# Optimization experiments

Measured on AMD Instinct MI355X. Metric: run time of the kernel, lower is better.

The kernel has to match this reference:

```python
import jax, jax.numpy as jnp
import numpy as np

SMALL = -1000.0


def setup_inputs() -> dict:
    key = jax.random.key(0)
    k1, k2, k3, k4 = jax.random.split(key, 4)
    B, T, L = 256, 1024, 64
    pred = jax.random.normal(k1, (B, T, L), dtype=jnp.float32)
    seq_len = jax.random.randint(k2, (B,), T // 2, T + 1)  # lengths in [T/2, T]
    ref = jax.random.randint(k3, (B, T), 0, L)
    # zero-pad tags beyond seq_len (required by the original end-tag indexing trick)
    ref = jnp.where(jnp.arange(T)[None, :] < seq_len[:, None], ref, 0)
    transitions = jax.random.normal(k4, (L + 2, L + 2), dtype=jnp.float32) * 0.1
    return {"pred": pred, "transitions": transitions, "ref": ref, "seq_len": seq_len}


def crf_neg_log_likelihood(pred, transitions, ref, seq_len):
    B, T, L = pred.shape
    dt = pred.dtype
    # --- build padded observations [B, T+2, L+2] ---
    obs_mid = jnp.concatenate([pred, jnp.full((B, T, 2), SMALL, dt)], axis=2)
    b_s = jnp.concatenate([jnp.full((L,), SMALL), jnp.array([0.0, SMALL])]).astype(dt)
    r_p = jnp.concatenate([jnp.zeros((L,)), jnp.array([SMALL, SMALL])]).astype(dt)
    obs = jnp.concatenate(
        [jnp.broadcast_to(b_s, (B, 1, L + 2)), obs_mid, jnp.broadcast_to(r_p, (B, 1, L + 2))],
        axis=1,
    )
    e_s = jnp.concatenate([jnp.full((L,), SMALL), jnp.array([0.0, 1000.0])]).astype(dt)
    obs = obs.at[jnp.arange(B), seq_len + 1].add(e_s)

    # --- forward algorithm: logsumexp recurrence over time ---
    def step(prev, ob):  # prev [B, L+2], ob [B, L+2]
        new = jax.nn.logsumexp(prev[:, :, None] + ob[:, None, :] + transitions[None], axis=1)
        return new, new

    prev0 = obs[:, 0]
    obs_t = jnp.swapaxes(obs[:, 1:], 0, 1)  # [T+1, B, L+2] time-major
    _, paths = jax.lax.scan(step, prev0, obs_t)  # paths [T+1, B, L+2]
    all_paths_scores = jax.nn.logsumexp(paths[seq_len, jnp.arange(B)], axis=1).sum()

    # --- gold path score ---
    mask = (jnp.arange(T)[None, :] < seq_len[:, None]).astype(dt)
    gold_emit = jnp.sum(jnp.take_along_axis(pred, ref[..., None], axis=2)[..., 0] * mask)
    padded = jnp.concatenate(
        [jnp.full((B, 1), L, ref.dtype), ref, jnp.zeros((B, 1), ref.dtype)], axis=1
    )  # [B, T+2]
    padded = padded.at[jnp.arange(B), seq_len + 1].add(L + 1)  # end tag id = L+1
    trans_sc = transitions[padded[:, :-1], padded[:, 1:]]  # [B, T+1]
    mask2 = (jnp.arange(T + 1)[None, :] < (seq_len + 1)[:, None]).astype(dt)
    gold = gold_emit + jnp.sum(trans_sc * mask2)
    return all_paths_scores - gold


def reference(pred, transitions, ref, seq_len):
    return crf_neg_log_likelihood(pred, transitions, ref, seq_len)
```

## Files before the change

### kernel.cpp

```cpp
#include <hip/hip_runtime.h>
#include <hip/hip_bf16.h>
#include <hip/hip_fp16.h>


typedef _Float16 h2 __attribute__((ext_vector_type(2)));
#define B2U(x) __builtin_bit_cast(unsigned, x)
#define U2H(x) __builtin_bit_cast(h2, x)
#define L2E 1.44269504088896340736f
#define LN2 0.69314718055994530942f
#define EXPE(p) __builtin_amdgcn_exp2f((p) * L2E)
#define SBAR __builtin_amdgcn_sched_barrier(0)

#define W_ALL(M) M(0) M(1) M(2) M(3) M(4) M(5) M(6) M(7) M(8) M(9) M(10) M(11) \
 M(12) M(13) M(14) M(15) M(16) M(17) M(18) M(19) M(20) M(21) M(22) M(23) M(24) \
 M(25) M(26) M(27) M(28) M(29) M(30) M(31)

#define DECLW(q) unsigned W##q;
#define LOADF(q) W##q = B2U(__builtin_amdgcn_cvt_pkrtz(EXPE(tcol[(2*(q))*66]), EXPE(tcol[(2*(q)+1)*66])));
#define LOADB(q) W##q = B2U(__builtin_amdgcn_cvt_pkrtz(EXPE(trow[2*(q)]), EXPE(trow[2*(q)+1])));
#define PINW(q)  asm volatile("" : "+v"(W##q));

#define RLD(q) int u##q = __builtin_amdgcn_readlane((int)P, 2*(q));
#define RL16A RLD(0) RLD(1) RLD(2) RLD(3) RLD(4) RLD(5) RLD(6) RLD(7) \
              RLD(8) RLD(9) RLD(10) RLD(11) RLD(12) RLD(13) RLD(14) RLD(15)
#define RL16B RLD(16) RLD(17) RLD(18) RLD(19) RLD(20) RLD(21) RLD(22) RLD(23) \
              RLD(24) RLD(25) RLD(26) RLD(27) RLD(28) RLD(29) RLD(30) RLD(31)

#if __has_builtin(__builtin_amdgcn_fdot2)
#define DOTQ(q, acc) acc = __builtin_amdgcn_fdot2(U2H((unsigned)u##q), U2H(W##q), acc, false);
#else
#define DOTQ(q, acc) { h2 _u = U2H((unsigned)u##q), _w = U2H(W##q); \
    acc = fmaf((float)_u[0], (float)_w[0], fmaf((float)_u[1], (float)_w[1], acc)); }
#endif
#define DOT16A \
    DOTQ(0,s0)  DOTQ(1,s1)  DOTQ(2,s2)  DOTQ(3,s3)  DOTQ(4,s0)  DOTQ(5,s1) \
    DOTQ(6,s2)  DOTQ(7,s3)  DOTQ(8,s0)  DOTQ(9,s1)  DOTQ(10,s2) DOTQ(11,s3) \
    DOTQ(12,s0) DOTQ(13,s1) DOTQ(14,s2) DOTQ(15,s3)
#define DOT16B \
    DOTQ(16,s0) DOTQ(17,s1) DOTQ(18,s2) DOTQ(19,s3) DOTQ(20,s0) DOTQ(21,s1) \
    DOTQ(22,s2) DOTQ(23,s3) DOTQ(24,s0) DOTQ(25,s1) DOTQ(26,s2) DOTQ(27,s3) \
    DOTQ(28,s0) DOTQ(29,s1) DOTQ(30,s2) DOTQ(31,s3)

#define ROWF(i) pb[(((i) < 0) ? 0 : (((i) > 1023) ? 1023 : (i))) * 64]

#define DPPSWAP(x) __uint_as_float((unsigned)__builtin_amdgcn_mov_dpp( \
    (int)__float_as_uint(x), 0xB1, 0xF, 0xF, true))

#define STEPX(E) { \
    unsigned abits = (unsigned)__builtin_amdgcn_readfirstlane((int)__float_as_uint(a)); \
    int k = (int)((abits >> 23) & 255u) - 122; \
    K += k; \
    float sc = __uint_as_float((unsigned)(127 - k) << 23); \
    float x = FWD ? a * sc : (a * sc) * (E); \
    float xo = DPPSWAP(x); \
    unsigned P = B2U(__builtin_amdgcn_cvt_pkrtz(x, xo)); \
    float s0 = 0.f, s1 = 0.f, s2 = 0.f, s3 = 0.f; \
    RL16A \
    SBAR; \
    DOT16A \
    RL16B \
    SBAR; \
    DOT16B \
    float s = (s0 + s1) + (s2 + s3); \
    a = FWD ? s * (E) : s; }

template<bool FWD>
__device__ __forceinline__ void chain(const float* __restrict__ pred,
                                      const float* __restrict__ trans,
                                      int b, int lane, int sl, int h,
                                      float* __restrict__ wsV,
                                      int* __restrict__ wsK)
{
    const float* pb   = pred + (size_t)b * 65536 + lane;
    const float* tcol = trans + lane;
    const float* trow = trans + lane * 66;
    (void)tcol; (void)trow;

    W_ALL(DECLW)
    if (FWD) { W_ALL(LOADF) } else { W_ALL(LOADB) }
    W_ALL(PINW)

    float a;
    int   K = 0;
    if (FWD) a = __builtin_amdgcn_exp2f((pb[0] + trans[64 * 66 + lane]) * L2E);
    else     a = __builtin_amdgcn_exp2f(trow[65] * L2E);

    const int dir = FWD ? 1 : -1;
    int n = FWD ? h - 1 : sl - h;
    int r = FWD ? 1 : sl - 1;

    float E0 = EXPE(ROWF(r)), E1 = EXPE(ROWF(r + dir)),
          E2 = EXPE(ROWF(r + 2 * dir)), E3 = EXPE(ROWF(r + 3 * dir));
    while (n >= 4) {
        float F0 = ROWF(r + 4 * dir), F1 = ROWF(r + 5 * dir),
              F2 = ROWF(r + 6 * dir), F3 = ROWF(r + 7 * dir);
        STEPX(E0) STEPX(E1) STEPX(E2) STEPX(E3)
        E0 = EXPE(F0); E1 = EXPE(F1); E2 = EXPE(F2); E3 = EXPE(F3);
        r += 4 * dir; n -= 4;
    }
    if (n > 0) { STEPX(E0) --n; }
    if (n > 0) { STEPX(E1) --n; }
    if (n > 0) { STEPX(E2) }

    wsV[b * 64 + lane] = a;
    if (lane == 0) wsK[b] = K;
}

__global__ __launch_bounds__(64) __attribute__((amdgpu_waves_per_eu(1, 1)))
void chain_kernel(const float* __restrict__ pred,
                  const float* __restrict__ trans,
                  const int*   __restrict__ ref,
                  const int*   __restrict__ seqlen,
                  float* __restrict__ wsA, float* __restrict__ wsB,
                  int* __restrict__ wsKf, int* __restrict__ wsKb,
                  float* __restrict__ out)
{
    const int role = blockIdx.x >> 8;
    const int b    = blockIdx.x & 255;
    const int lane = threadIdx.x;
    const int sl   = seqlen[b];
    const int h    = (sl + 1) >> 1;

    if (role == 0) {
        chain<true>(pred, trans, b, lane, sl, h, wsA, wsKf);
    } else if (role == 1) {
        chain<false>(pred, trans, b, lane, sl, h, wsB, wsKb);
    } else {
        const int*   rb = ref  + b * 1024;
        const float* pg = pred + (size_t)b * 65536;
        float acc = 0.f;
        for (int t = lane; t <= sl; t += 64) {
            int from = (t == 0) ? 64 : rb[t - 1];
            int cur  = (t < sl) ? rb[t] : 65;
            acc += trans[from * 66 + cur];
            if (t < sl) acc += pg[t * 64 + cur];
        }
        #pragma unroll
        for (int off = 32; off; off >>= 1) acc += __shfl_xor(acc, off, 64);
        if (lane == 0) atomicAdd(out, -acc);
    }
}

__global__ __launch_bounds__(64) void combine_kernel(
    const float* __restrict__ wsA, const float* __restrict__ wsB,
    const int* __restrict__ wsKf, const int* __restrict__ wsKb,
    float* __restrict__ out)
{
    const int b = blockIdx.x, lane = threadIdx.x;
    float z = wsA[b * 64 + lane] * wsB[b * 64 + lane];
    #pragma unroll
    for (int off = 32; off; off >>= 1) z += __shfl_xor(z, off, 64);
    if (lane == 0) {
        float res = LN2 * (__builtin_amdgcn_logf(z) + (float)(wsKf[b] + wsKb[b]));
        atomicAdd(out, res);
    }
}

extern "C" void kernel_launch(void* const* d_in, const int* in_sizes, int n_in,
                              void* d_out, int out_size, void* d_ws, size_t ws_size,
                              hipStream_t stream) {
    const float* pred   = (const float*)d_in[0];
    const float* trans  = (const float*)d_in[1];
    const int*   ref    = (const int*)d_in[2];
    const int*   seqlen = (const int*)d_in[3];
    float* out = (float*)d_out;

    float* wsA  = (float*)d_ws;
    float* wsB  = wsA + 256 * 64;
    int*   wsKf = (int*)(wsB + 256 * 64);
    int*   wsKb = wsKf + 256;

    hipMemsetAsync(out, 0, sizeof(float), stream);
    chain_kernel<<<768, 64, 0, stream>>>(pred, trans, ref, seqlen,
                                         wsA, wsB, wsKf, wsKb, out);
    combine_kernel<<<256, 64, 0, stream>>>(wsA, wsB, wsKf, wsKb, out);
}
```

Before: 182.0 us.

## Split CRF forward chain into parallel 128-step transfer-matrix segments via MFMA

Instead of a forward and a backward chain each covering half the sequence, the sequence is cut into 128-step segments. The middle segments are computed in parallel as products of 64x64 exp-transition matrices using fp16 MFMA, with per-step power-of-two rescaling. The forward chain covers the first 128 steps and the backward chain covers the tail. The combine kernel then chains the segment matrices as matrix-vector products. This shortens the serial dependency chain from about sl/2 steps to about 128, but adds matrix-matrix work, fp16 precision loss in the matrix products, and workspace traffic.

```diff
diff --git a/kernel.cpp b/kernel.cpp
--- a/kernel.cpp
+++ b/kernel.cpp
@@ -4,12 +4,18 @@
 
 
 typedef _Float16 h2 __attribute__((ext_vector_type(2)));
+typedef _Float16 half8 __attribute__((ext_vector_type(8)));
+typedef float f32x16 __attribute__((ext_vector_type(16)));
+typedef unsigned u32x2 __attribute__((ext_vector_type(2)));
+typedef unsigned u32x4 __attribute__((ext_vector_type(4)));
+
 #define B2U(x) __builtin_bit_cast(unsigned, x)
 #define U2H(x) __builtin_bit_cast(h2, x)
 #define L2E 1.44269504088896340736f
 #define LN2 0.69314718055994530942f
 #define EXPE(p) __builtin_amdgcn_exp2f((p) * L2E)
 #define SBAR __builtin_amdgcn_sched_barrier(0)
+
 
 #define W_ALL(M) M(0) M(1) M(2) M(3) M(4) M(5) M(6) M(7) M(8) M(9) M(10) M(11) \
  M(12) M(13) M(14) M(15) M(16) M(17) M(18) M(19) M(20) M(21) M(22) M(23) M(24) \
@@ -106,26 +112,135 @@
     if (lane == 0) wsK[b] = K;
 }
 
-__global__ __launch_bounds__(64) __attribute__((amdgpu_waves_per_eu(1, 1)))
+
+#define MFMA16(a, b, c) __builtin_amdgcn_mfma_f32_32x32x16_f16(a, b, c, 0, 0, 0)
+
+#define PACKGRP(Csrc, base, dst) { \
+    unsigned q0 = B2U(__builtin_amdgcn_cvt_pkrtz(Csrc[(base)+0], Csrc[(base)+1])); \
+    unsigned q2 = B2U(__builtin_amdgcn_cvt_pkrtz(Csrc[(base)+2], Csrc[(base)+3])); \
+    unsigned q4 = B2U(__builtin_amdgcn_cvt_pkrtz(Csrc[(base)+4], Csrc[(base)+5])); \
+    unsigned q6 = B2U(__builtin_amdgcn_cvt_pkrtz(Csrc[(base)+6], Csrc[(base)+7])); \
+    asm("v_permlane32_swap_b32 %0, %1" : "+v"(q0), "+v"(q4)); \
+    asm("v_permlane32_swap_b32 %0, %1" : "+v"(q2), "+v"(q6)); \
+    u32x4 qv = {q0, q2, q4, q6}; \
+    dst = __builtin_bit_cast(half8, qv); }
+
+#define STORET(Ct, t4) { \
+    _Pragma("unroll") \
+    for (int g = 0; g < 4; ++g) { \
+        u32x2 pv; \
+        pv.x = B2U(__builtin_amdgcn_cvt_pkrtz(Ct[4*g+0], Ct[4*g+1])); \
+        pv.y = B2U(__builtin_amdgcn_cvt_pkrtz(Ct[4*g+2], Ct[4*g+3])); \
+        *(u32x2*)(wm + (t4)*1024 + g*256 + lane*4) = pv; } }
+
+__device__ __forceinline__ void midseg(const float* __restrict__ pred,
+                                       const float* __restrict__ trans,
+                                       int b, int lane, int sl, int s,
+                                       _Float16* __restrict__ wsM,
+                                       int* __restrict__ wsKm)
+{
+    const int nm = (sl - 128) >> 7;
+    if (s >= nm) return;
+    const int t0 = 128 * (1 + s);
+    const int H  = lane >> 5;
+    const int j0 = lane & 31;
+
+    half8 VA[2][4];
+    #pragma unroll
+    for (int mt = 0; mt < 2; ++mt)
+        #pragma unroll
+        for (int s4 = 0; s4 < 4; ++s4) {
+            half8 va;
+            #pragma unroll
+            for (int e = 0; e < 8; ++e) {
+                int k = 16 * s4 + 8 * H + e;
+                va[e] = (_Float16)EXPE(trans[k * 66 + 32 * mt + j0]);
+            }
+            VA[mt][s4] = va;
+        }
+
+    half8 Bf[4][2];
+    #pragma unroll
+    for (int s4 = 0; s4 < 4; ++s4)
+        #pragma unroll
+        for (int nt = 0; nt < 2; ++nt) {
+            half8 bb;
+            #pragma unroll
+            for (int e = 0; e < 8; ++e)
+                bb[e] = (16 * s4 + 8 * H + e == 32 * nt + j0) ? (_Float16)1.f
+                                                              : (_Float16)0.f;
+            Bf[s4][nt] = bb;
+        }
+
+    const float* pp = pred + (size_t)b * 65536 + j0;
+    float a0 = pp[(size_t)t0 * 64],        a1 = pp[(size_t)t0 * 64 + 32];
+    float q0 = pp[(size_t)(t0 + 1) * 64],  q1 = pp[(size_t)(t0 + 1) * 64 + 32];
+
+    const f32x16 Z16 = {0.f,0.f,0.f,0.f,0.f,0.f,0.f,0.f,
+                        0.f,0.f,0.f,0.f,0.f,0.f,0.f,0.f};
+    f32x16 C00 = Z16, C01 = Z16, C10 = Z16, C11 = Z16;
+    int   K   = 0;
+    float scf = 1.0f;
+
+    for (int i = 0; i < 128; ++i) {
+        int tn = t0 + i + 2; if (tn > 1023) tn = 1023;
+        float n0 = pp[(size_t)tn * 64], n1 = pp[(size_t)tn * 64 + 32];
+
+        if (i > 0) {
+            float sr = ((C00[0]+C00[1])+(C00[2]+C00[3]))+((C00[4]+C00[5])+(C00[6]+C00[7]))
+                     + ((C00[8]+C00[9])+(C00[10]+C00[11]))+((C00[12]+C00[13])+(C00[14]+C00[15]));
+            unsigned cb = (unsigned)__builtin_amdgcn_readfirstlane((int)__float_as_uint(sr));
+            int kk = (int)((cb >> 23) & 255u) - 129;
+            K += kk;
+            scf = __uint_as_float((unsigned)(127 - kk) << 23);
+            PACKGRP(C00, 0, Bf[0][0]) PACKGRP(C00, 8, Bf[1][0])
+            PACKGRP(C10, 0, Bf[2][0]) PACKGRP(C10, 8, Bf[3][0])
+            PACKGRP(C01, 0, Bf[0][1]) PACKGRP(C01, 8, Bf[1][1])
+            PACKGRP(C11, 0, Bf[2][1]) PACKGRP(C11, 8, Bf[3][1])
+        }
+        float e0 = EXPE(a0) * scf, e1 = EXPE(a1) * scf;
+        _Float16 h0 = (_Float16)e0, h1 = (_Float16)e1;
+        half8 E0v = {h0,h0,h0,h0,h0,h0,h0,h0};
+        half8 E1v = {h1,h1,h1,h1,h1,h1,h1,h1};
+        half8 A00 = VA[0][0]*E0v, A01 = VA[0][1]*E0v, A02 = VA[0][2]*E0v, A03 = VA[0][3]*E0v;
+        half8 A10 = VA[1][0]*E1v, A11 = VA[1][1]*E1v, A12 = VA[1][2]*E1v, A13 = VA[1][3]*E1v;
+
+        C00 = MFMA16(A00, Bf[0][0], MFMA16(A01, Bf[1][0], MFMA16(A02, Bf[2][0], MFMA16(A03, Bf[3][0], Z16))));
+        C01 = MFMA16(A00, Bf[0][1], MFMA16(A01, Bf[1][1], MFMA16(A02, Bf[2][1], MFMA16(A03, Bf[3][1], Z16))));
+        C10 = MFMA16(A10, Bf[0][0], MFMA16(A11, Bf[1][0], MFMA16(A12, Bf[2][0], MFMA16(A13, Bf[3][0], Z16))));
+        C11 = MFMA16(A10, Bf[0][1], MFMA16(A11, Bf[1][1], MFMA16(A12, Bf[2][1], MFMA16(A13, Bf[3][1], Z16))));
+
+        a0 = q0; a1 = q1; q0 = n0; q1 = n1;
+    }
+
+    _Float16* wm = wsM + (size_t)(b * 7 + s) * 4096;
+    STORET(C00, 0) STORET(C01, 1) STORET(C10, 2) STORET(C11, 3)
+    if (lane == 0) wsKm[b * 7 + s] = K;
+}
+
+
+__global__ __launch_bounds__(64) __attribute__((amdgpu_waves_per_eu(2)))
 void chain_kernel(const float* __restrict__ pred,
                   const float* __restrict__ trans,
                   const int*   __restrict__ ref,
                   const int*   __restrict__ seqlen,
                   float* __restrict__ wsA, float* __restrict__ wsB,
                   int* __restrict__ wsKf, int* __restrict__ wsKb,
+                  _Float16* __restrict__ wsM, int* __restrict__ wsKm,
                   float* __restrict__ out)
 {
     const int role = blockIdx.x >> 8;
     const int b    = blockIdx.x & 255;
     const int lane = threadIdx.x;
     const int sl   = seqlen[b];
-    const int h    = (sl + 1) >> 1;
 
     if (role == 0) {
-        chain<true>(pred, trans, b, lane, sl, h, wsA, wsKf);
+        chain<true>(pred, trans, b, lane, sl, 128, wsA, wsKf);
     } else if (role == 1) {
-        chain<false>(pred, trans, b, lane, sl, h, wsB, wsKb);
-    } else {
+        const int nm = (sl - 128) >> 7;
+        const int tb = 128 * (1 + nm);
+        chain<false>(pred, trans, b, lane, sl, tb, wsB, wsKb);
+    } else if (role == 2) {
         const int*   rb = ref  + b * 1024;
         const float* pg = pred + (size_t)b * 65536;
         float acc = 0.f;
@@ -138,20 +253,50 @@
         #pragma unroll
         for (int off = 32; off; off >>= 1) acc += __shfl_xor(acc, off, 64);
         if (lane == 0) atomicAdd(out, -acc);
+    } else {
+        midseg(pred, trans, b, lane, sl, role - 3, wsM, wsKm);
     }
 }
 
 __global__ __launch_bounds__(64) void combine_kernel(
     const float* __restrict__ wsA, const float* __restrict__ wsB,
+    const _Float16* __restrict__ wsM,
     const int* __restrict__ wsKf, const int* __restrict__ wsKb,
+    const int* __restrict__ wsKm, const int* __restrict__ seqlen,
     float* __restrict__ out)
 {
-    const int b = blockIdx.x, lane = threadIdx.x;
-    float z = wsA[b * 64 + lane] * wsB[b * 64 + lane];
+    const int b = blockIdx.x, j = threadIdx.x;
+    const int sl = seqlen[b];
+    const int nm = (sl - 128) >> 7;
+
+    float v = wsA[b * 64 + j];
+    int   K = wsKf[b] + wsKb[b];
+
+    const int mt = j >> 5, hi = (j >> 2) & 1, g = (j >> 3) & 3, e = j & 3;
+    const _Float16* mb = wsM + (size_t)b * 7 * 4096 + mt * 2048 + g * 256 + hi * 128 + e;
+
+    for (int s = 0; s < nm; ++s) {
+        K += wsKm[b * 7 + s];
+        const _Float16* ms = mb + (size_t)s * 4096;
+        float acc = 0.f;
+        #pragma unroll
+        for (int c = 0; c < 64; ++c) {
+            float m  = (float)ms[(c >> 5) * 1024 + (c & 31) * 4];
+            float vc = __uint_as_float(
+                (unsigned)__builtin_amdgcn_readlane((int)__float_as_uint(v), c));
+            acc = fmaf(m, vc, acc);
+        }
+        unsigned ab = (unsigned)__builtin_amdgcn_readfirstlane((int)__float_as_uint(acc));
+        int k2 = (int)((ab >> 23) & 255u) - 127;
+        K += k2;
+        v = acc * __uint_as_float((unsigned)(127 - k2) << 23);
+    }
+
+    float z = v * wsB[b * 64 + j];
     #pragma unroll
     for (int off = 32; off; off >>= 1) z += __shfl_xor(z, off, 64);
-    if (lane == 0) {
-        float res = LN2 * (__builtin_amdgcn_logf(z) + (float)(wsKf[b] + wsKb[b]));
+    if (j == 0) {
+        float res = LN2 * (__builtin_amdgcn_logf(z) + (float)K);
         atomicAdd(out, res);
     }
 }
@@ -169,9 +314,12 @@
     float* wsB  = wsA + 256 * 64;
     int*   wsKf = (int*)(wsB + 256 * 64);
     int*   wsKb = wsKf + 256;
+    int*   wsKm = wsKb + 256;
+    _Float16* wsM = (_Float16*)(wsKm + 256 * 7);
 
     hipMemsetAsync(out, 0, sizeof(float), stream);
-    chain_kernel<<<768, 64, 0, stream>>>(pred, trans, ref, seqlen,
-                                         wsA, wsB, wsKf, wsKb, out);
-    combine_kernel<<<256, 64, 0, stream>>>(wsA, wsB, wsKf, wsKb, out);
-}
+    chain_kernel<<<2560, 64, 0, stream>>>(pred, trans, ref, seqlen,
+                                          wsA, wsB, wsKf, wsKb, wsM, wsKm, out);
+    combine_kernel<<<256, 64, 0, stream>>>(wsA, wsB, wsM, wsKf, wsKb, wsKm,
+                                           seqlen, out);
+}
```

New measurement: 227.3 us. +24.9%, slower.

## Split CRF forward chain into parallel MFMA transfer-matrix segments

Applied to the files above, without the earlier changes.

The forward chain now covers only the first G steps and the backward chain only the tail. The middle is cut into segments of G steps, and each segment gets its own block. That block computes a 64x64 transfer-matrix product with fp16 MFMA, rescaling by exponent each step. A combine kernel then chains the segment matrices with the forward vector. This replaces the long serial per-batch recurrence with parallel segments that are serial only over G. In exchange it adds heavier matrix-matrix work, an fp16 precision risk, and a larger workspace, with a fallback configuration when the workspace is too small.

```diff
diff --git a/kernel.cpp b/kernel.cpp
--- a/kernel.cpp
+++ b/kernel.cpp
@@ -4,12 +4,18 @@
 
 
 typedef _Float16 h2 __attribute__((ext_vector_type(2)));
+typedef _Float16 half4v __attribute__((ext_vector_type(4)));
+typedef float f32x4 __attribute__((ext_vector_type(4)));
+typedef unsigned u32x2 __attribute__((ext_vector_type(2)));
+typedef unsigned u32x4 __attribute__((ext_vector_type(4)));
+
 #define B2U(x) __builtin_bit_cast(unsigned, x)
 #define U2H(x) __builtin_bit_cast(h2, x)
 #define L2E 1.44269504088896340736f
 #define LN2 0.69314718055994530942f
 #define EXPE(p) __builtin_amdgcn_exp2f((p) * L2E)
 #define SBAR __builtin_amdgcn_sched_barrier(0)
+
 
 #define W_ALL(M) M(0) M(1) M(2) M(3) M(4) M(5) M(6) M(7) M(8) M(9) M(10) M(11) \
  M(12) M(13) M(14) M(15) M(16) M(17) M(18) M(19) M(20) M(21) M(22) M(23) M(24) \
@@ -106,26 +112,155 @@
     if (lane == 0) wsK[b] = K;
 }
 
-__global__ __launch_bounds__(64) __attribute__((amdgpu_waves_per_eu(1, 1)))
+
+#define MF16(a, b, c) __builtin_amdgcn_mfma_f32_16x16x16f16(a, b, c, 0, 0, 0)
+
+#define MKE(es) __builtin_bit_cast(half4v, (u32x2){ \
+    B2U(__builtin_amdgcn_cvt_pkrtz((es), (es))), \
+    B2U(__builtin_amdgcn_cvt_pkrtz((es), (es))) })
+
+#define MBROW(mb, EV) { \
+    half4v A0 = VA[mb][0]*(EV), A1 = VA[mb][1]*(EV), \
+           A2 = VA[mb][2]*(EV), A3 = VA[mb][3]*(EV); \
+    _Pragma("unroll") \
+    for (int nb = 0; nb < 4; ++nb) { \
+        f32x4 acc = {0.f, 0.f, 0.f, 0.f}; \
+        acc = MF16(A0, Bf[0][nb], acc); \
+        acc = MF16(A1, Bf[1][nb], acc); \
+        acc = MF16(A2, Bf[2][nb], acc); \
+        acc = MF16(A3, Bf[3][nb], acc); \
+        Cn[mb][nb] = acc; } }
+
+template<int LOGG, int NSLOT>
+__device__ __forceinline__ void midseg(const float* __restrict__ pred,
+                                       const float* __restrict__ trans,
+                                       int b, int lane, int sl, int s,
+                                       _Float16* __restrict__ wsM,
+                                       int* __restrict__ wsKm)
+{
+    const int G  = 1 << LOGG;
+    const int nm = (sl - G) >> LOGG;
+    if (s >= nm) return;
+    const int t0 = G * (1 + s);
+    const int H  = lane >> 4;
+    const int j0 = lane & 15;
+
+    half4v VA[4][4];
+    #pragma unroll
+    for (int mb = 0; mb < 4; ++mb)
+        #pragma unroll
+        for (int kb = 0; kb < 4; ++kb) {
+            const float* tp = trans + (16*kb + 4*H) * 66 + 16*mb + j0;
+            u32x2 q;
+            q.x = B2U(__builtin_amdgcn_cvt_pkrtz(EXPE(tp[0]),   EXPE(tp[66])));
+            q.y = B2U(__builtin_amdgcn_cvt_pkrtz(EXPE(tp[132]), EXPE(tp[198])));
+            VA[mb][kb] = __builtin_bit_cast(half4v, q);
+        }
+
+    half4v Bf[4][4];
+    #pragma unroll
+    for (int kb = 0; kb < 4; ++kb)
+        #pragma unroll
+        for (int nb = 0; nb < 4; ++nb) {
+            half4v bb;
+            #pragma unroll
+            for (int e = 0; e < 4; ++e)
+                bb[e] = (16*kb + 4*H + e == 16*nb + j0) ? (_Float16)1.f
+                                                        : (_Float16)0.f;
+            Bf[kb][nb] = bb;
+        }
+
+    const float* pp = pred + (size_t)b * 65536 + j0;
+    float eA0 = EXPE(pp[(size_t)t0*64]),      eA1 = EXPE(pp[(size_t)t0*64+16]),
+          eA2 = EXPE(pp[(size_t)t0*64+32]),   eA3 = EXPE(pp[(size_t)t0*64+48]);
+    float eB0 = EXPE(pp[(size_t)(t0+1)*64]),    eB1 = EXPE(pp[(size_t)(t0+1)*64+16]),
+          eB2 = EXPE(pp[(size_t)(t0+1)*64+32]), eB3 = EXPE(pp[(size_t)(t0+1)*64+48]);
+
+    f32x4 C[4][4];
+    #pragma unroll
+    for (int mb = 0; mb < 4; ++mb)
+        #pragma unroll
+        for (int nb = 0; nb < 4; ++nb)
+            C[mb][nb] = (f32x4){0.f, 0.f, 0.f, 0.f};
+
+    int   K   = 0;
+    float scf = 1.0f;
+
+    for (int i = 0; i < G; ++i) {
+        int tn = t0 + i + 2; if (tn > 1023) tn = 1023;
+        float g0 = pp[(size_t)tn*64],    g1 = pp[(size_t)tn*64+16],
+              g2 = pp[(size_t)tn*64+32], g3 = pp[(size_t)tn*64+48];
+
+        if (i > 0) {
+            float sr = ((C[0][0][0]+C[0][0][1])+(C[0][0][2]+C[0][0][3]))
+                     + ((C[1][0][0]+C[1][0][1])+(C[1][0][2]+C[1][0][3]))
+                     + ((C[2][0][0]+C[2][0][1])+(C[2][0][2]+C[2][0][3]))
+                     + ((C[3][0][0]+C[3][0][1])+(C[3][0][2]+C[3][0][3]));
+            unsigned cb = (unsigned)__builtin_amdgcn_readfirstlane((int)__float_as_uint(sr));
+            int kk = (int)((cb >> 23) & 255u) - 129;
+            K += kk;
+            scf = __uint_as_float((unsigned)(127 - kk) << 23);
+            #pragma unroll
+            for (int kb = 0; kb < 4; ++kb)
+                #pragma unroll
+                for (int nb = 0; nb < 4; ++nb) {
+                    u32x2 q;
+                    q.x = B2U(__builtin_amdgcn_cvt_pkrtz(C[kb][nb][0], C[kb][nb][1]));
+                    q.y = B2U(__builtin_amdgcn_cvt_pkrtz(C[kb][nb][2], C[kb][nb][3]));
+                    Bf[kb][nb] = __builtin_bit_cast(half4v, q);
+                }
+        }
+
+        float es0 = eA0*scf, es1 = eA1*scf, es2 = eA2*scf, es3 = eA3*scf;
+        half4v E0 = MKE(es0), E1 = MKE(es1), E2 = MKE(es2), E3 = MKE(es3);
+
+        f32x4 Cn[4][4];
+        MBROW(0, E0) MBROW(1, E1) MBROW(2, E2) MBROW(3, E3)
+        #pragma unroll
+        for (int mb = 0; mb < 4; ++mb)
+            #pragma unroll
+            for (int nb = 0; nb < 4; ++nb)
+                C[mb][nb] = Cn[mb][nb];
+
+        eA0 = eB0; eA1 = eB1; eA2 = eB2; eA3 = eB3;
+        eB0 = EXPE(g0); eB1 = EXPE(g1); eB2 = EXPE(g2); eB3 = EXPE(g3);
+    }
+
+    _Float16* wm = wsM + ((size_t)b * NSLOT + s) * 4096;
+    #pragma unroll
+    for (int mb = 0; mb < 4; ++mb)
+        #pragma unroll
+        for (int nb = 0; nb < 4; ++nb)
+            #pragma unroll
+            for (int r = 0; r < 4; ++r)
+                wm[(16*mb + 4*H + r) * 64 + 16*nb + j0] = (_Float16)C[mb][nb][r];
+    if (lane == 0) wsKm[b * NSLOT + s] = K;
+}
+
+
+template<int LOGG, int NSLOT>
+__global__ __launch_bounds__(64)
 void chain_kernel(const float* __restrict__ pred,
                   const float* __restrict__ trans,
                   const int*   __restrict__ ref,
                   const int*   __restrict__ seqlen,
                   float* __restrict__ wsA, float* __restrict__ wsB,
                   int* __restrict__ wsKf, int* __restrict__ wsKb,
+                  _Float16* __restrict__ wsM, int* __restrict__ wsKm,
                   float* __restrict__ out)
 {
     const int role = blockIdx.x >> 8;
     const int b    = blockIdx.x & 255;
     const int lane = threadIdx.x;
     const int sl   = seqlen[b];
-    const int h    = (sl + 1) >> 1;
+    const int G    = 1 << LOGG;
 
     if (role == 0) {
-        chain<true>(pred, trans, b, lane, sl, h, wsA, wsKf);
+        chain<true>(pred, trans, b, lane, sl, G, wsA, wsKf);
     } else if (role == 1) {
-        chain<false>(pred, trans, b, lane, sl, h, wsB, wsKb);
-    } else {
+        const int nm = (sl - G) >> LOGG;
+        chain<false>(pred, trans, b, lane, sl, G * (1 + nm), wsB, wsKb);
+    } else if (role == 2) {
         const int*   rb = ref  + b * 1024;
         const float* pg = pred + (size_t)b * 65536;
         float acc = 0.f;
@@ -138,22 +273,80 @@
         #pragma unroll
         for (int off = 32; off; off >>= 1) acc += __shfl_xor(acc, off, 64);
         if (lane == 0) atomicAdd(out, -acc);
-    }
-}
-
+    } else {
+        midseg<LOGG, NSLOT>(pred, trans, b, lane, sl, role - 3, wsM, wsKm);
+    }
+}
+
+template<int LOGG, int NSLOT>
 __global__ __launch_bounds__(64) void combine_kernel(
     const float* __restrict__ wsA, const float* __restrict__ wsB,
+    const _Float16* __restrict__ wsM,
     const int* __restrict__ wsKf, const int* __restrict__ wsKb,
+    const int* __restrict__ wsKm, const int* __restrict__ seqlen,
     float* __restrict__ out)
 {
-    const int b = blockIdx.x, lane = threadIdx.x;
-    float z = wsA[b * 64 + lane] * wsB[b * 64 + lane];
+    const int b = blockIdx.x, j = threadIdx.x;
+    const int sl = seqlen[b];
+    const int nm = (sl - (1 << LOGG)) >> LOGG;
+
+    float v = wsA[b * 64 + j];
+    int   K = wsKf[b] + wsKb[b];
+    const _Float16* mrow = wsM + (size_t)b * NSLOT * 4096 + j * 64;
+
+    for (int s = 0; s < nm; ++s) {
+        K += wsKm[b * NSLOT + s];
+        const u32x4* mp = (const u32x4*)(mrow + (size_t)s * 4096);
+        u32x4 L0 = mp[0], L1 = mp[1], L2 = mp[2], L3 = mp[3],
+              L4 = mp[4], L5 = mp[5], L6 = mp[6], L7 = mp[7];
+        unsigned mw[32] = {L0.x,L0.y,L0.z,L0.w, L1.x,L1.y,L1.z,L1.w,
+                           L2.x,L2.y,L2.z,L2.w, L3.x,L3.y,L3.z,L3.w,
+                           L4.x,L4.y,L4.z,L4.w, L5.x,L5.y,L5.z,L5.w,
+                           L6.x,L6.y,L6.z,L6.w, L7.x,L7.y,L7.z,L7.w};
+        float av[4] = {0.f, 0.f, 0.f, 0.f};
+        #pragma unroll
+        for (int q = 0; q < 32; ++q) {
+            h2 p = U2H(mw[q]);
+            float v0 = __uint_as_float((unsigned)
+                __builtin_amdgcn_readlane((int)__float_as_uint(v), 2*q));
+            float v1 = __uint_as_float((unsigned)
+                __builtin_amdgcn_readlane((int)__float_as_uint(v), 2*q + 1));
+            av[q & 3] = fmaf((float)p[0], v0, fmaf((float)p[1], v1, av[q & 3]));
+        }
+        float acc = (av[0] + av[1]) + (av[2] + av[3]);
+        unsigned ab = (unsigned)__builtin_amdgcn_readfirstlane((int)__float_as_uint(acc));
+        int k2 = (int)((ab >> 23) & 255u) - 127;
+        K += k2;
+        v = acc * __uint_as_float((unsigned)(127 - k2) << 23);
+    }
+
+    float z = v * wsB[b * 64 + j];
     #pragma unroll
     for (int off = 32; off; off >>= 1) z += __shfl_xor(z, off, 64);
-    if (lane == 0) {
-        float res = LN2 * (__builtin_amdgcn_logf(z) + (float)(wsKf[b] + wsKb[b]));
+    if (j == 0) {
+        float res = LN2 * (__builtin_amdgcn_logf(z) + (float)K);
         atomicAdd(out, res);
     }
+}
+
+
+template<int LOGG, int NSLOT>
+static void launch_all(const float* pred, const float* trans, const int* ref,
+                       const int* seqlen, float* out, void* d_ws,
+                       hipStream_t stream)
+{
+    float* wsA  = (float*)d_ws;
+    float* wsB  = wsA + 256 * 64;
+    int*   wsKf = (int*)(wsB + 256 * 64);
+    int*   wsKb = wsKf + 256;
+    int*   wsKm = wsKb + 256;
+    _Float16* wsM = (_Float16*)(wsKm + 256 * NSLOT);
+
+    hipMemsetAsync(out, 0, sizeof(float), stream);
+    chain_kernel<LOGG, NSLOT><<<256 * (3 + NSLOT), 64, 0, stream>>>(
+        pred, trans, ref, seqlen, wsA, wsB, wsKf, wsKb, wsM, wsKm, out);
+    combine_kernel<LOGG, NSLOT><<<256, 64, 0, stream>>>(
+        wsA, wsB, wsM, wsKf, wsKb, wsKm, seqlen, out);
 }
 
 extern "C" void kernel_launch(void* const* d_in, const int* in_sizes, int n_in,
@@ -165,13 +358,10 @@
     const int*   seqlen = (const int*)d_in[3];
     float* out = (float*)d_out;
 
-    float* wsA  = (float*)d_ws;
-    float* wsB  = wsA + 256 * 64;
-    int*   wsKf = (int*)(wsB + 256 * 64);
-    int*   wsKb = wsKf + 256;
-
-    hipMemsetAsync(out, 0, sizeof(float), stream);
-    chain_kernel<<<768, 64, 0, stream>>>(pred, trans, ref, seqlen,
-                                         wsA, wsB, wsKf, wsKb, out);
-    combine_kernel<<<256, 64, 0, stream>>>(wsA, wsB, wsKf, wsKb, out);
-}
+    const size_t need64 = 2*65536 + 2*1024 + (size_t)256*15*4
+                        + (size_t)256*15*4096*2;
+    if (ws_size >= need64)
+        launch_all<6, 15>(pred, trans, ref, seqlen, out, d_ws, stream);
+    else
+        launch_all<7, 7>(pred, trans, ref, seqlen, out, d_ws, stream);
+}
```

Measured after the change: 255.1 us. +40.2%, slower.

## Replace readlane/fdot2 recurrence with MFMA 16x16x32 matrix-vector steps

Applied to the files above, without the earlier changes.

The per-step 64x64 matrix-vector product of the forward/backward CRF chains is now computed with MFMA f16 instructions. exp(transitions) is held as A fragments, and the state vector is broadcast as a B operand with identical columns. This removes the 32 readlane plus 32 fdot2 sequence per step, but adds MFMA latency on the serial dependency chain. The scaling now uses a sum of the 16 per-lane state values, and the emissions are loaded as float4 slices in the MFMA output layout.

```diff
diff --git a/kernel.cpp b/kernel.cpp
--- a/kernel.cpp
+++ b/kernel.cpp
@@ -1,108 +1,138 @@
 #include <hip/hip_runtime.h>
-#include <hip/hip_bf16.h>
 #include <hip/hip_fp16.h>
 
 
 typedef _Float16 h2 __attribute__((ext_vector_type(2)));
+typedef _Float16 half8 __attribute__((ext_vector_type(8)));
+typedef float f32x4 __attribute__((ext_vector_type(4)));
+typedef unsigned u32x4 __attribute__((ext_vector_type(4)));
+
 #define B2U(x) __builtin_bit_cast(unsigned, x)
-#define U2H(x) __builtin_bit_cast(h2, x)
 #define L2E 1.44269504088896340736f
 #define LN2 0.69314718055994530942f
 #define EXPE(p) __builtin_amdgcn_exp2f((p) * L2E)
-#define SBAR __builtin_amdgcn_sched_barrier(0)
-
-#define W_ALL(M) M(0) M(1) M(2) M(3) M(4) M(5) M(6) M(7) M(8) M(9) M(10) M(11) \
- M(12) M(13) M(14) M(15) M(16) M(17) M(18) M(19) M(20) M(21) M(22) M(23) M(24) \
- M(25) M(26) M(27) M(28) M(29) M(30) M(31)
-
-#define DECLW(q) unsigned W##q;
-#define LOADF(q) W##q = B2U(__builtin_amdgcn_cvt_pkrtz(EXPE(tcol[(2*(q))*66]), EXPE(tcol[(2*(q)+1)*66])));
-#define LOADB(q) W##q = B2U(__builtin_amdgcn_cvt_pkrtz(EXPE(trow[2*(q)]), EXPE(trow[2*(q)+1])));
-#define PINW(q)  asm volatile("" : "+v"(W##q));
-
-#define RLD(q) int u##q = __builtin_amdgcn_readlane((int)P, 2*(q));
-#define RL16A RLD(0) RLD(1) RLD(2) RLD(3) RLD(4) RLD(5) RLD(6) RLD(7) \
-              RLD(8) RLD(9) RLD(10) RLD(11) RLD(12) RLD(13) RLD(14) RLD(15)
-#define RL16B RLD(16) RLD(17) RLD(18) RLD(19) RLD(20) RLD(21) RLD(22) RLD(23) \
-              RLD(24) RLD(25) RLD(26) RLD(27) RLD(28) RLD(29) RLD(30) RLD(31)
-
-#if __has_builtin(__builtin_amdgcn_fdot2)
-#define DOTQ(q, acc) acc = __builtin_amdgcn_fdot2(U2H((unsigned)u##q), U2H(W##q), acc, false);
-#else
-#define DOTQ(q, acc) { h2 _u = U2H((unsigned)u##q), _w = U2H(W##q); \
-    acc = fmaf((float)_u[0], (float)_w[0], fmaf((float)_u[1], (float)_w[1], acc)); }
-#endif
-#define DOT16A \
-    DOTQ(0,s0)  DOTQ(1,s1)  DOTQ(2,s2)  DOTQ(3,s3)  DOTQ(4,s0)  DOTQ(5,s1) \
-    DOTQ(6,s2)  DOTQ(7,s3)  DOTQ(8,s0)  DOTQ(9,s1)  DOTQ(10,s2) DOTQ(11,s3) \
-    DOTQ(12,s0) DOTQ(13,s1) DOTQ(14,s2) DOTQ(15,s3)
-#define DOT16B \
-    DOTQ(16,s0) DOTQ(17,s1) DOTQ(18,s2) DOTQ(19,s3) DOTQ(20,s0) DOTQ(21,s1) \
-    DOTQ(22,s2) DOTQ(23,s3) DOTQ(24,s0) DOTQ(25,s1) DOTQ(26,s2) DOTQ(27,s3) \
-    DOTQ(28,s0) DOTQ(29,s1) DOTQ(30,s2) DOTQ(31,s3)
-
-#define ROWF(i) pb[(((i) < 0) ? 0 : (((i) > 1023) ? 1023 : (i))) * 64]
-
-#define DPPSWAP(x) __uint_as_float((unsigned)__builtin_amdgcn_mov_dpp( \
-    (int)__float_as_uint(x), 0xB1, 0xF, 0xF, true))
-
-#define STEPX(E) { \
-    unsigned abits = (unsigned)__builtin_amdgcn_readfirstlane((int)__float_as_uint(a)); \
-    int k = (int)((abits >> 23) & 255u) - 122; \
-    K += k; \
-    float sc = __uint_as_float((unsigned)(127 - k) << 23); \
-    float x = FWD ? a * sc : (a * sc) * (E); \
-    float xo = DPPSWAP(x); \
-    unsigned P = B2U(__builtin_amdgcn_cvt_pkrtz(x, xo)); \
-    float s0 = 0.f, s1 = 0.f, s2 = 0.f, s3 = 0.f; \
-    RL16A \
-    SBAR; \
-    DOT16A \
-    RL16B \
-    SBAR; \
-    DOT16B \
-    float s = (s0 + s1) + (s2 + s3); \
-    a = FWD ? s * (E) : s; }
+#define MF32(a, b, c) __builtin_amdgcn_mfma_f32_16x16x32_f16(a, b, c, 0, 0, 0)
+
+#define KG(ks, H, e) (32*(ks) + (((e) < 4) ? (4*(H) + (e)) : (16 + 4*(H) + (e) - 4)))
 
 template<bool FWD>
-__device__ __forceinline__ void chain(const float* __restrict__ pred,
-                                      const float* __restrict__ trans,
-                                      int b, int lane, int sl, int h,
-                                      float* __restrict__ wsV,
-                                      int* __restrict__ wsK)
+__device__ __forceinline__ void chainM(const float* __restrict__ pred,
+                                       const float* __restrict__ trans,
+                                       int b, int lane, int sl, int h,
+                                       float* __restrict__ wsV,
+                                       int* __restrict__ wsK)
 {
-    const float* pb   = pred + (size_t)b * 65536 + lane;
-    const float* tcol = trans + lane;
-    const float* trow = trans + lane * 66;
-    (void)tcol; (void)trow;
-
-    W_ALL(DECLW)
-    if (FWD) { W_ALL(LOADF) } else { W_ALL(LOADB) }
-    W_ALL(PINW)
-
-    float a;
-    int   K = 0;
-    if (FWD) a = __builtin_amdgcn_exp2f((pb[0] + trans[64 * 66 + lane]) * L2E);
-    else     a = __builtin_amdgcn_exp2f(trow[65] * L2E);
-
+    const int H  = lane >> 4;
+    const int j0 = lane & 15;
+    const f32x4 Z4 = {0.f, 0.f, 0.f, 0.f};
+    const float* pb = pred + (size_t)b * 65536;
+
+    half8 VA[4][2];
+    #pragma unroll
+    for (int mb = 0; mb < 4; ++mb)
+        #pragma unroll
+        for (int ks = 0; ks < 2; ++ks) {
+            u32x4 q;
+            if (FWD) {
+                const float* tp = trans + 16*mb + j0;
+                q.x = B2U(__builtin_amdgcn_cvt_pkrtz(EXPE(tp[KG(ks,H,0)*66]), EXPE(tp[KG(ks,H,1)*66])));
+                q.y = B2U(__builtin_amdgcn_cvt_pkrtz(EXPE(tp[KG(ks,H,2)*66]), EXPE(tp[KG(ks,H,3)*66])));
+                q.z = B2U(__builtin_amdgcn_cvt_pkrtz(EXPE(tp[KG(ks,H,4)*66]), EXPE(tp[KG(ks,H,5)*66])));
+                q.w = B2U(__builtin_amdgcn_cvt_pkrtz(EXPE(tp[KG(ks,H,6)*66]), EXPE(tp[KG(ks,H,7)*66])));
+            } else {
+                const float* tp = trans + (16*mb + j0) * 66;
+                q.x = B2U(__builtin_amdgcn_cvt_pkrtz(EXPE(tp[KG(ks,H,0)]), EXPE(tp[KG(ks,H,1)])));
+                q.y = B2U(__builtin_amdgcn_cvt_pkrtz(EXPE(tp[KG(ks,H,2)]), EXPE(tp[KG(ks,H,3)])));
+                q.z = B2U(__builtin_amdgcn_cvt_pkrtz(EXPE(tp[KG(ks,H,4)]), EXPE(tp[KG(ks,H,5)])));
+                q.w = B2U(__builtin_amdgcn_cvt_pkrtz(EXPE(tp[KG(ks,H,6)]), EXPE(tp[KG(ks,H,7)])));
+            }
+            VA[mb][ks] = __builtin_bit_cast(half8, q);
+        }
+
+    f32x4 C[4];
+    #pragma unroll
+    for (int a = 0; a < 4; ++a)
+        #pragma unroll
+        for (int r = 0; r < 4; ++r) {
+            int m = 16*a + 4*H + r;
+            C[a][r] = FWD ? EXPE(pb[m] + trans[64*66 + m])
+                          : EXPE(trans[m*66 + 65]);
+        }
+
+    int K = 0;
+    int n = FWD ? h - 1 : sl - h;
+    int t = FWD ? 1 : sl - 1;
     const int dir = FWD ? 1 : -1;
-    int n = FWD ? h - 1 : sl - h;
-    int r = FWD ? 1 : sl - 1;
-
-    float E0 = EXPE(ROWF(r)), E1 = EXPE(ROWF(r + dir)),
-          E2 = EXPE(ROWF(r + 2 * dir)), E3 = EXPE(ROWF(r + 3 * dir));
-    while (n >= 4) {
-        float F0 = ROWF(r + 4 * dir), F1 = ROWF(r + 5 * dir),
-              F2 = ROWF(r + 6 * dir), F3 = ROWF(r + 7 * dir);
-        STEPX(E0) STEPX(E1) STEPX(E2) STEPX(E3)
-        E0 = EXPE(F0); E1 = EXPE(F1); E2 = EXPE(F2); E3 = EXPE(F3);
-        r += 4 * dir; n -= 4;
-    }
-    if (n > 0) { STEPX(E0) --n; }
-    if (n > 0) { STEPX(E1) --n; }
-    if (n > 0) { STEPX(E2) }
-
-    wsV[b * 64 + lane] = a;
+
+    const float* pt = pb + (size_t)t * 64 + 4*H;
+    f32x4 PE[4] = { *(const f32x4*)(pt +  0), *(const f32x4*)(pt + 16),
+                    *(const f32x4*)(pt + 32), *(const f32x4*)(pt + 48) };
+
+    while (n > 0) {
+        const float* pn = pb + (size_t)(t + dir) * 64 + 4*H;
+        f32x4 P0 = *(const f32x4*)(pn +  0), P1 = *(const f32x4*)(pn + 16),
+              P2 = *(const f32x4*)(pn + 32), P3 = *(const f32x4*)(pn + 48);
+
+        f32x4 EX[4];
+        #pragma unroll
+        for (int a = 0; a < 4; ++a) {
+            EX[a][0] = EXPE(PE[a][0]); EX[a][1] = EXPE(PE[a][1]);
+            EX[a][2] = EXPE(PE[a][2]); EX[a][3] = EXPE(PE[a][3]);
+        }
+
+        float sr = ((C[0][0]+C[0][1])+(C[0][2]+C[0][3]))
+                 + ((C[1][0]+C[1][1])+(C[1][2]+C[1][3]))
+                 + ((C[2][0]+C[2][1])+(C[2][2]+C[2][3]))
+                 + ((C[3][0]+C[3][1])+(C[3][2]+C[3][3]));
+        unsigned cb = (unsigned)__builtin_amdgcn_readfirstlane((int)__float_as_uint(sr));
+        int kk = (int)((cb >> 23) & 255u) - 129;
+        K += kk;
+        float sc = __uint_as_float((unsigned)(127 - kk) << 23);
+
+        f32x4 Tv[4];
+        #pragma unroll
+        for (int a = 0; a < 4; ++a) {
+            if (FWD) {
+                Tv[a][0]=C[a][0]*sc; Tv[a][1]=C[a][1]*sc;
+                Tv[a][2]=C[a][2]*sc; Tv[a][3]=C[a][3]*sc;
+            } else {
+                Tv[a][0]=C[a][0]*(EX[a][0]*sc); Tv[a][1]=C[a][1]*(EX[a][1]*sc);
+                Tv[a][2]=C[a][2]*(EX[a][2]*sc); Tv[a][3]=C[a][3]*(EX[a][3]*sc);
+            }
+        }
+        u32x4 qb0, qb1;
+        qb0.x = B2U(__builtin_amdgcn_cvt_pkrtz(Tv[0][0], Tv[0][1]));
+        qb0.y = B2U(__builtin_amdgcn_cvt_pkrtz(Tv[0][2], Tv[0][3]));
+        qb0.z = B2U(__builtin_amdgcn_cvt_pkrtz(Tv[1][0], Tv[1][1]));
+        qb0.w = B2U(__builtin_amdgcn_cvt_pkrtz(Tv[1][2], Tv[1][3]));
+        qb1.x = B2U(__builtin_amdgcn_cvt_pkrtz(Tv[2][0], Tv[2][1]));
+        qb1.y = B2U(__builtin_amdgcn_cvt_pkrtz(Tv[2][2], Tv[2][3]));
+        qb1.z = B2U(__builtin_amdgcn_cvt_pkrtz(Tv[3][0], Tv[3][1]));
+        qb1.w = B2U(__builtin_amdgcn_cvt_pkrtz(Tv[3][2], Tv[3][3]));
+        half8 Bf0 = __builtin_bit_cast(half8, qb0);
+        half8 Bf1 = __builtin_bit_cast(half8, qb1);
+
+        #pragma unroll
+        for (int mb = 0; mb < 4; ++mb) {
+            f32x4 acc = MF32(VA[mb][0], Bf0, Z4);
+            acc = MF32(VA[mb][1], Bf1, acc);
+            if (FWD) {
+                C[mb][0] = acc[0]*EX[mb][0]; C[mb][1] = acc[1]*EX[mb][1];
+                C[mb][2] = acc[2]*EX[mb][2]; C[mb][3] = acc[3]*EX[mb][3];
+            } else {
+                C[mb] = acc;
+            }
+        }
+
+        PE[0] = P0; PE[1] = P1; PE[2] = P2; PE[3] = P3;
+        t += dir; --n;
+    }
+
+    if (j0 == 0) {
+        #pragma unroll
+        for (int mb = 0; mb < 4; ++mb)
+            *(f32x4*)(wsV + b * 64 + 16*mb + 4*H) = C[mb];
+    }
     if (lane == 0) wsK[b] = K;
 }
 
@@ -122,9 +152,9 @@
     const int h    = (sl + 1) >> 1;
 
     if (role == 0) {
-        chain<true>(pred, trans, b, lane, sl, h, wsA, wsKf);
+        chainM<true>(pred, trans, b, lane, sl, h, wsA, wsKf);
     } else if (role == 1) {
-        chain<false>(pred, trans, b, lane, sl, h, wsB, wsKb);
+        chainM<false>(pred, trans, b, lane, sl, h, wsB, wsKb);
     } else {
         const int*   rb = ref  + b * 1024;
         const float* pg = pred + (size_t)b * 65536;
```

Measured after the change: 382.0 us. 110% more time.
